# Performance work log

Hardware: AMD Instinct MI355X
Metric: run time of the kernel (lower is better)

The kernel has to match this reference:

```python
import jax, jax.numpy as jnp
import numpy as np

B, C, H, W = 4, 256, 64, 64
D_STATE, D_CONV, EXPAND = 16, 4, 2
D_INNER = EXPAND * C          # 512
DT_RANK = (C + 15) // 16      # 16 (math.ceil(d_model/16), mamba_ssm default)


def setup_inputs() -> dict:
    key = jax.random.key(0)
    ks = jax.random.split(key, 16)
    s = lambda k, shp, sc=0.02: (jax.random.normal(k, shp, dtype=jnp.float32) * sc)
    inp = {
        "spatial_feat": jax.random.normal(ks[0], (B, C, H, W), dtype=jnp.float32),
        "freq_feat":    jax.random.normal(ks[1], (B, C, H, W), dtype=jnp.float32),
        # fusion proj: Linear(2C -> C)
        "W_proj": s(ks[2], (C, 2 * C)),
        "b_proj": jnp.zeros((C,), jnp.float32),
        # Mamba params (mamba_ssm defaults: bias=False for in/out proj, conv_bias=True)
        "W_in":   s(ks[3], (2 * D_INNER, C)),
        "conv_w": s(ks[4], (D_INNER, 1, D_CONV), 0.1),
        "conv_b": jnp.zeros((D_INNER,), jnp.float32),
        "W_x":    s(ks[5], (DT_RANK + 2 * D_STATE, D_INNER)),
        "W_dt":   s(ks[6], (D_INNER, DT_RANK), 0.1),
        "b_dt":   s(ks[7], (D_INNER,), 0.5),
        "A_log":  jnp.log(jnp.tile(jnp.arange(1, D_STATE + 1, dtype=jnp.float32), (D_INNER, 1))),
        "D":      jnp.ones((D_INNER,), jnp.float32),
        "W_out":  s(ks[8], (C, D_INNER)),
        # LayerNorm
        "ln_gamma": jnp.ones((C,), jnp.float32),
        "ln_beta":  jnp.zeros((C,), jnp.float32),
    }
    return inp


def _mamba(x, W_in, conv_w, conv_b, W_x, W_dt, b_dt, A_log, Dp, W_out):
    # x: [B, L, C]
    Bb, L, _ = x.shape
    xz = jnp.einsum("blc,ec->ble", x, W_in)              # [B,L,2*d_inner]
    u, z = jnp.split(xz, 2, axis=-1)                      # each [B,L,d_inner]
    # causal depthwise conv1d along L
    u_c = jnp.transpose(u, (0, 2, 1))                     # [B,d_inner,L]
    u_c = jax.lax.conv_general_dilated(
        u_c, conv_w, window_strides=(1,), padding=[(D_CONV - 1, 0)],
        dimension_numbers=("NCH", "OIH", "NCH"), feature_group_count=D_INNER)
    u_c = u_c + conv_b[None, :, None]
    u = jax.nn.silu(jnp.transpose(u_c, (0, 2, 1)))        # [B,L,d_inner]
    # input-dependent dt, B, C
    dbc = jnp.einsum("bld,rd->blr", u, W_x)               # [B,L,dt_rank+2*d_state]
    dt = dbc[..., :DT_RANK]
    Bm = dbc[..., DT_RANK:DT_RANK + D_STATE]              # [B,L,d_state]
    Cm = dbc[..., DT_RANK + D_STATE:]                     # [B,L,d_state]
    delta = jax.nn.softplus(jnp.einsum("blr,dr->bld", dt, W_dt) + b_dt)  # [B,L,d_inner]
    A = -jnp.exp(A_log)                                   # [d_inner,d_state]

    def step(h, t):
        delta_t, B_t, C_t, u_t = t                        # [B,di],[B,ds],[B,ds],[B,di]
        dA = jnp.exp(delta_t[..., None] * A)              # [B,di,ds]
        h = h * dA + (delta_t * u_t)[..., None] * B_t[:, None, :]
        y = jnp.einsum("bds,bs->bd", h, C_t)
        return h, y

    tm = lambda a: jnp.swapaxes(a, 0, 1)                  # [B,L,..] -> [L,B,..]
    h0 = jnp.zeros((Bb, D_INNER, D_STATE), x.dtype)
    _, ys = jax.lax.scan(step, h0, (tm(delta), tm(Bm), tm(Cm), tm(u)))
    y = jnp.swapaxes(ys, 0, 1)                            # [B,L,d_inner]
    y = y + u * Dp
    y = y * jax.nn.silu(z)
    return jnp.einsum("bld,cd->blc", y, W_out)            # [B,L,C]


def reference(spatial_feat, freq_feat, W_proj, b_proj, W_in, conv_w, conv_b,
              W_x, W_dt, b_dt, A_log, D, W_out, ln_gamma, ln_beta):
    Bb, Cc, Hh, Ww = spatial_feat.shape
    L = Hh * Ww
    xs = jnp.transpose(spatial_feat.reshape(Bb, Cc, L), (0, 2, 1))  # [B,L,C]
    xf = jnp.transpose(freq_feat.reshape(Bb, Cc, L), (0, 2, 1))
    x_cat = jnp.concatenate([xs, xf], axis=-1)                       # [B,L,2C]
    x_proj = jnp.einsum("ble,ce->blc", x_cat, W_proj) + b_proj       # [B,L,C]
    x_mixed = _mamba(x_proj, W_in, conv_w, conv_b, W_x, W_dt, b_dt, A_log, D, W_out)
    mu = jnp.mean(x_mixed, axis=-1, keepdims=True)
    var = jnp.var(x_mixed, axis=-1, keepdims=True)
    x_out = (x_mixed - mu) * jax.lax.rsqrt(var + 1e-5) * ln_gamma + ln_beta
    return jnp.transpose(x_out, (0, 2, 1)).reshape(Bb, Cc, Hh, Ww)
```

## Files before the change

### kernel.cpp

```cpp
#include <hip/hip_runtime.h>
#include <hip/hip_fp16.h>
#include <math.h>

#define L 4096
#define CDIM 256
#define DIN 512
#define DSTATE 16
#define DTR 16
#define BATCH 4

using f32x4  = __attribute__((ext_vector_type(4))) float;
using f16x8  = __attribute__((ext_vector_type(8))) _Float16;

#define LOG2E 1.44269504088896f

#if __has_builtin(__builtin_amdgcn_exp2f)
#define EXP2(x) __builtin_amdgcn_exp2f(x)
#else
#define EXP2(x) __expf((x) * 0.69314718056f)
#endif

__device__ __forceinline__ float silu_f(float x) {
    return __fdividef(x, 1.f + __expf(-x));
}
__device__ __forceinline__ float softplus_fast(float x) {
    return (x > 20.f) ? x : __logf(1.f + __expf(x));
}
__device__ __forceinline__ unsigned pk2h(float a, float b) {
    __half2 h = __floats2half2_rn(a, b);
    return *reinterpret_cast<unsigned*>(&h);
}

#define LDK 40

enum { HEPI_XP = 0, HEPI_UZ = 1, HEPI_F32 = 2, HEPI_D34 = 3 };
template<int EPI, bool A_F32KM, int NT>
__global__ __launch_bounds__(256)
void hgemm(const float* __restrict__ Af0, const float* __restrict__ Af1,
           const __half* __restrict__ Ah_g, const __half* __restrict__ Bh_g,
           const float* __restrict__ bias,
           float* __restrict__ O0, __half* __restrict__ Oh0, __half* __restrict__ Oh1,
           float* __restrict__ Ob, float* __restrict__ Oc,
           int M, int N, int K, int kSplit, long strideAb, int nBlk)
{
    constexpr int BM = 64, MT = 2;
    constexpr int BN = 2 * NT * 16;
    constexpr int BSEG = BN / 64;
    __shared__ __align__(16) _Float16 Ah[2][BM][LDK];
    __shared__ __align__(16) _Float16 Bh[2][BN][LDK];
    const int mBlk = M / BM;
    const int bid = blockIdx.x;
    const int r = bid & 7, q = bid >> 3;
    const int ni = q % nBlk;
    const int mg = (q / nBlk) * 8 + r;
    const int b = mg / mBlk, m_idx = mg - b * mBlk;
    const int n0 = ni * BN, m0 = m_idx * BM;
    const int tid  = threadIdx.x;
    const int lane = tid & 63;
    const int w    = tid >> 6;
    const int wr   = w >> 1, wc = w & 1;
    const int lrow = lane & 15;
    const int loct = lane >> 4;

    f32x4 acc[MT][NT];
    #pragma unroll
    for (int i = 0; i < MT; ++i)
        #pragma unroll
        for (int j = 0; j < NT; ++j)
            acc[i][j] = (f32x4){0.f, 0.f, 0.f, 0.f};

    const int sOct = tid & 3, sRow = tid >> 2;
    float va[8];
    uint4 pa, pb[BSEG];

    auto loadA = [&](int kk) {
        if (A_F32KM) {
            int m = tid & 63, ks = tid >> 6;
            #pragma unroll
            for (int j = 0; j < 8; ++j) {
                int kg = kk + ks * 8 + j;
                const float* Ap; int kl;
                if (kg < kSplit) { Ap = Af0; kl = kg; } else { Ap = Af1; kl = kg - kSplit; }
                va[j] = Ap[(long)b * strideAb + (long)kl * M + m0 + m];
            }
        } else {
            pa = *(const uint4*)(Ah_g + (long)b * strideAb +
                                 (long)(m0 + sRow) * K + kk + sOct * 8);
        }
    };
    auto loadB = [&](int kk) {
        #pragma unroll
        for (int p = 0; p < BSEG; ++p) {
            int ng = n0 + sRow + p * 64;
            if (EPI == HEPI_D34 && ng >= N)
                pb[p] = make_uint4(0, 0, 0, 0);
            else
                pb[p] = *(const uint4*)(Bh_g + (long)ng * K + kk + sOct * 8);
        }
    };
    auto storeAB = [&](int buf) {
        if (A_F32KM) {
            int m = tid & 63, ks = tid >> 6;
            uint4 h;
            h.x = pk2h(va[0], va[1]);
            h.y = pk2h(va[2], va[3]);
            h.z = pk2h(va[4], va[5]);
            h.w = pk2h(va[6], va[7]);
            *(uint4*)&Ah[buf][m][ks * 8] = h;
        } else {
            *(uint4*)&Ah[buf][sRow][sOct * 8] = pa;
        }
        #pragma unroll
        for (int p = 0; p < BSEG; ++p)
            *(uint4*)&Bh[buf][sRow + p * 64][sOct * 8] = pb[p];
    };

    loadA(0); loadB(0);
    storeAB(0);
    __syncthreads();
    int cur = 0;
    for (int kk = 0; kk < K; kk += 32) {
        const bool more = (kk + 32 < K);
        if (more) { loadA(kk + 32); loadB(kk + 32); }
        f16x8 bh[NT];
        #pragma unroll
        for (int nt = 0; nt < NT; ++nt)
            bh[nt] = *(const f16x8*)&Bh[cur][wc*NT*16 + nt*16 + lrow][loct*8];
        #pragma unroll
        for (int mt = 0; mt < MT; ++mt) {
            f16x8 ah = *(const f16x8*)&Ah[cur][wr*MT*16 + mt*16 + lrow][loct*8];
            #pragma unroll
            for (int nt = 0; nt < NT; ++nt)
                acc[mt][nt] = __builtin_amdgcn_mfma_f32_16x16x32_f16(ah, bh[nt], acc[mt][nt], 0, 0, 0);
        }
        if (more) {
            storeAB(cur ^ 1);
            __syncthreads();
            cur ^= 1;
        }
    }
    #pragma unroll
    for (int mt = 0; mt < MT; ++mt) {
        #pragma unroll
        for (int r4 = 0; r4 < 4; ++r4) {
            int m = m0 + wr*MT*16 + mt * 16 + loct * 4 + r4;
            long rowb = (long)b * M + m;
            #pragma unroll
            for (int nt = 0; nt < NT; ++nt) {
                int n = n0 + wc*NT*16 + nt * 16 + lrow;
                float v = acc[mt][nt][r4];
                if (EPI == HEPI_XP) {
                    Oh0[rowb * N + n] = __float2half(v + bias[n]);
                } else if (EPI == HEPI_UZ) {
                    if (n < DIN) Oh0[rowb * DIN + n] = __float2half(v);
                    else         Oh1[rowb * DIN + (n - DIN)] = __float2half(v);
                } else if (EPI == HEPI_D34) {
                    if (n < DTR)           O0[rowb * DTR + n] = v;
                    else if (n < 2 * DTR)  Ob[rowb * 16 + (n - DTR)] = v;
                    else if (n < 48)       Oc[rowb * 16 + (n - 32)] = v;
                } else {
                    O0[rowb * N + n] = v;
                }
            }
        }
    }
}

#define SZ_WP  131072
#define SZ_WIN 262144
#define SZ_WO  131072
#define SZ_WC  24576
__global__ __launch_bounds__(256)
void pack_all(const float* __restrict__ Wp, const float* __restrict__ Win,
              const float* __restrict__ Wout, const float* __restrict__ Wx,
              __half* __restrict__ wph, __half* __restrict__ winh,
              __half* __restrict__ woh, __half* __restrict__ wch)
{
    int i = blockIdx.x * 256 + threadIdx.x;
    if (i < SZ_WP) { wph[i] = __float2half(Wp[i]); return; }
    i -= SZ_WP;
    if (i < SZ_WIN) { winh[i] = __float2half(Win[i]); return; }
    i -= SZ_WIN;
    if (i < SZ_WO) { woh[i] = __float2half(Wout[i]); return; }
    i -= SZ_WO;
    if (i < SZ_WC) wch[i] = __float2half(Wx[i]);
}

__global__ __launch_bounds__(256)
void conv_silu_kernel(const __half* __restrict__ u_pre, const float* __restrict__ cw,
                      const float* __restrict__ cb, __half* __restrict__ u)
{
    long idx = (long)blockIdx.x * blockDim.x + threadIdx.x;
    int d = (int)(idx % DIN);
    long bl = idx / DIN;
    int l = (int)(bl % L);
    long brow = bl - l;
    float v = cb[d];
    #pragma unroll
    for (int j = 0; j < 4; ++j) {
        int li = l - 3 + j;
        if (li >= 0) v += __half2float(u_pre[(brow + li) * DIN + d]) * cw[d * 4 + j];
    }
    u[idx] = __float2half(silu_f(v));
}

#define NC 128
#define LC (L / NC)

__global__ __launch_bounds__(256)
void scan_phase1(const float* __restrict__ dtA, const __half* __restrict__ u,
                 const float* __restrict__ Bm, const float* __restrict__ A_log,
                 const float* __restrict__ Wdt, const float* __restrict__ bdt,
                 float* __restrict__ AX)
{
    __shared__ float sB[LC][DSTATE];
    __shared__ float sDt[LC][DTR];
    __shared__ __half sU[LC][256];
    const int gd = blockIdx.x & 1;
    const int c  = (blockIdx.x >> 1) & (NC - 1);
    const int b  = blockIdx.x >> 8;
    const int tid = threadIdx.x;
    const int d  = gd * 256 + tid;
    const int t0 = c * LC;
    float Arow[DSTATE];
    #pragma unroll
    for (int q = 0; q < 4; ++q) {
        float4 v = *(const float4*)&A_log[d * DSTATE + q * 4];
        Arow[q * 4 + 0] = -__expf(v.x) * LOG2E;
        Arow[q * 4 + 1] = -__expf(v.y) * LOG2E;
        Arow[q * 4 + 2] = -__expf(v.z) * LOG2E;
        Arow[q * 4 + 3] = -__expf(v.w) * LOG2E;
    }
    const float4 W0 = *(const float4*)&Wdt[d * DTR + 0];
    const float4 W1 = *(const float4*)&Wdt[d * DTR + 4];
    const float4 W2 = *(const float4*)&Wdt[d * DTR + 8];
    const float4 W3 = *(const float4*)&Wdt[d * DTR + 12];
    const float bd = bdt[d];
    {
        const __half* ub = u + ((long)b * L + t0) * DIN + gd * 256;
        #pragma unroll
        for (int j = 0; j < 4; ++j) {
            int i = tid + j * 256;
            int t = i >> 5, col = (i & 31) * 8;
            *(float4*)&sU[t][col] = *(const float4*)&ub[(long)t * DIN + col];
        }
        if (tid < 128) {
            const float* Bb = Bm  + ((long)b * L + t0) * DSTATE;
            const float* Db = dtA + ((long)b * L + t0) * DTR;
            *(float4*)&((float*)sB)[tid * 4]  = *(const float4*)&Bb[tid * 4];
            *(float4*)&((float*)sDt)[tid * 4] = *(const float4*)&Db[tid * 4];
        }
    }
    __syncthreads();
    float P[DSTATE], X[DSTATE];
    #pragma unroll
    for (int s = 0; s < DSTATE; ++s) { P[s] = 1.f; X[s] = 0.f; }
    #pragma unroll 2
    for (int t = 0; t < LC; ++t) {
        float4 q0 = *(const float4*)&sDt[t][0];
        float4 q1 = *(const float4*)&sDt[t][4];
        float4 q2 = *(const float4*)&sDt[t][8];
        float4 q3 = *(const float4*)&sDt[t][12];
        float dp0 = fmaf(q0.x, W0.x, fmaf(q0.y, W0.y, fmaf(q0.z, W0.z, q0.w * W0.w)));
        float dp1 = fmaf(q1.x, W1.x, fmaf(q1.y, W1.y, fmaf(q1.z, W1.z, q1.w * W1.w)));
        float dp2 = fmaf(q2.x, W2.x, fmaf(q2.y, W2.y, fmaf(q2.z, W2.z, q2.w * W2.w)));
        float dp3 = fmaf(q3.x, W3.x, fmaf(q3.y, W3.y, fmaf(q3.z, W3.z, q3.w * W3.w)));
        float dlt = softplus_fast(((dp0 + dp1) + (dp2 + dp3)) + bd);
        float du  = dlt * __half2float(sU[t][tid]);
        float Brow[DSTATE];
        *(float4*)&Brow[0]  = *(const float4*)&sB[t][0];
        *(float4*)&Brow[4]  = *(const float4*)&sB[t][4];
        *(float4*)&Brow[8]  = *(const float4*)&sB[t][8];
        *(float4*)&Brow[12] = *(const float4*)&sB[t][12];
        #pragma unroll
        for (int s = 0; s < DSTATE; ++s) {
            float a = EXP2(dlt * Arow[s]);
            P[s] *= a;
            X[s] = fmaf(a, X[s], du * Brow[s]);
        }
    }
    long o2 = ((((long)b * NC + c) * DIN + d) * DSTATE) * 2;
    #pragma unroll
    for (int q = 0; q < 8; ++q)
        *(float4*)&AX[o2 + q * 4] =
            make_float4(P[2*q], X[2*q], P[2*q+1], X[2*q+1]);
}

__global__ __launch_bounds__(256)
void scan_phase2(const float* __restrict__ AX, float* __restrict__ Hout)
{
    int lane = blockIdx.x * 256 + threadIdx.x;
    int b = lane >> 13;
    int rem = lane & 8191;
    const long cs = (long)DIN * DSTATE;
    const long base = (long)b * NC * cs + rem;
    float h = 0.f;
    float2 c0, c1, c2, c3, n0, n1, n2, n3;
    auto ld = [&](int c) -> float2 {
        return *(const float2*)&AX[2 * (base + (long)c * cs)];
    };
    c0 = ld(0); c1 = ld(1); c2 = ld(2); c3 = ld(3);
    n0 = ld(4); n1 = ld(5); n2 = ld(6); n3 = ld(7);
    for (int c = 0; c < NC; c += 4) {
        Hout[base + (long)(c+0) * cs] = h; h = fmaf(c0.x, h, c0.y);
        Hout[base + (long)(c+1) * cs] = h; h = fmaf(c1.x, h, c1.y);
        Hout[base + (long)(c+2) * cs] = h; h = fmaf(c2.x, h, c2.y);
        Hout[base + (long)(c+3) * cs] = h; h = fmaf(c3.x, h, c3.y);
        c0 = n0; c1 = n1; c2 = n2; c3 = n3;
        if (c + 8 < NC) { n0 = ld(c+8); n1 = ld(c+9); n2 = ld(c+10); n3 = ld(c+11); }
    }
}

__global__ __launch_bounds__(256)
void scan_phase3(const float* __restrict__ dtA, const __half* __restrict__ u,
                 const float* __restrict__ Bm, const float* __restrict__ Cm,
                 const __half* __restrict__ z, const float* __restrict__ A_log,
                 const float* __restrict__ Wdt, const float* __restrict__ bdt,
                 const float* __restrict__ Dp, const float* __restrict__ Hinit,
                 __half* __restrict__ y2h)
{
    __shared__ float sB[LC][DSTATE], sC[LC][DSTATE];
    __shared__ float sDt[LC][DTR];
    __shared__ __half sU[LC][256];
    __shared__ __half sZ[LC][256];
    const int gd = blockIdx.x & 1;
    const int c  = (blockIdx.x >> 1) & (NC - 1);
    const int b  = blockIdx.x >> 8;
    const int tid = threadIdx.x;
    const int d  = gd * 256 + tid;
    const int t0 = c * LC;
    float Arow[DSTATE];
    #pragma unroll
    for (int q = 0; q < 4; ++q) {
        float4 v = *(const float4*)&A_log[d * DSTATE + q * 4];
        Arow[q * 4 + 0] = -__expf(v.x) * LOG2E;
        Arow[q * 4 + 1] = -__expf(v.y) * LOG2E;
        Arow[q * 4 + 2] = -__expf(v.z) * LOG2E;
        Arow[q * 4 + 3] = -__expf(v.w) * LOG2E;
    }
    const float4 W0 = *(const float4*)&Wdt[d * DTR + 0];
    const float4 W1 = *(const float4*)&Wdt[d * DTR + 4];
    const float4 W2 = *(const float4*)&Wdt[d * DTR + 8];
    const float4 W3 = *(const float4*)&Wdt[d * DTR + 12];
    const float bd = bdt[d];
    {
        const __half* ub = u + ((long)b * L + t0) * DIN + gd * 256;
        const __half* zb = z + ((long)b * L + t0) * DIN + gd * 256;
        #pragma unroll
        for (int j = 0; j < 4; ++j) {
            int i = tid + j * 256;
            int t = i >> 5, col = (i & 31) * 8;
            *(float4*)&sU[t][col] = *(const float4*)&ub[(long)t * DIN + col];
            *(float4*)&sZ[t][col] = *(const float4*)&zb[(long)t * DIN + col];
        }
        if (tid < 128) {
            const float* Bb = Bm  + ((long)b * L + t0) * DSTATE;
            const float* Cb = Cm  + ((long)b * L + t0) * DSTATE;
            const float* Db = dtA + ((long)b * L + t0) * DTR;
            *(float4*)&((float*)sB)[tid * 4]  = *(const float4*)&Bb[tid * 4];
            *(float4*)&((float*)sC)[tid * 4]  = *(const float4*)&Cb[tid * 4];
            *(float4*)&((float*)sDt)[tid * 4] = *(const float4*)&Db[tid * 4];
        }
    }
    float h[DSTATE];
    {
        long o = (((long)b * NC + c) * DIN + d) * DSTATE;
        #pragma unroll
        for (int q = 0; q < 4; ++q) {
            float4 v = *(const float4*)&Hinit[o + q * 4];
            h[q * 4 + 0] = v.x; h[q * 4 + 1] = v.y;
            h[q * 4 + 2] = v.z; h[q * 4 + 3] = v.w;
        }
    }
    const float Dval = Dp[d];
    __syncthreads();
    #pragma unroll 2
    for (int t = 0; t < LC; ++t) {
        float4 q0 = *(const float4*)&sDt[t][0];
        float4 q1 = *(const float4*)&sDt[t][4];
        float4 q2 = *(const float4*)&sDt[t][8];
        float4 q3 = *(const float4*)&sDt[t][12];
        float dp0 = fmaf(q0.x, W0.x, fmaf(q0.y, W0.y, fmaf(q0.z, W0.z, q0.w * W0.w)));
        float dp1 = fmaf(q1.x, W1.x, fmaf(q1.y, W1.y, fmaf(q1.z, W1.z, q1.w * W1.w)));
        float dp2 = fmaf(q2.x, W2.x, fmaf(q2.y, W2.y, fmaf(q2.z, W2.z, q2.w * W2.w)));
        float dp3 = fmaf(q3.x, W3.x, fmaf(q3.y, W3.y, fmaf(q3.z, W3.z, q3.w * W3.w)));
        float dlt = softplus_fast(((dp0 + dp1) + (dp2 + dp3)) + bd);
        float uu = __half2float(sU[t][tid]);
        float zz = __half2float(sZ[t][tid]);
        float du = dlt * uu;
        float Brow[DSTATE], Crow[DSTATE];
        *(float4*)&Brow[0]  = *(const float4*)&sB[t][0];
        *(float4*)&Brow[4]  = *(const float4*)&sB[t][4];
        *(float4*)&Brow[8]  = *(const float4*)&sB[t][8];
        *(float4*)&Brow[12] = *(const float4*)&sB[t][12];
        *(float4*)&Crow[0]  = *(const float4*)&sC[t][0];
        *(float4*)&Crow[4]  = *(const float4*)&sC[t][4];
        *(float4*)&Crow[8]  = *(const float4*)&sC[t][8];
        *(float4*)&Crow[12] = *(const float4*)&sC[t][12];
        float y0 = 0.f, y1 = 0.f, y2 = 0.f, y3 = 0.f;
        #pragma unroll
        for (int s = 0; s < DSTATE; s += 4) {
            float a0 = EXP2(dlt * Arow[s+0]);
            float a1 = EXP2(dlt * Arow[s+1]);
            float a2 = EXP2(dlt * Arow[s+2]);
            float a3 = EXP2(dlt * Arow[s+3]);
            h[s+0] = fmaf(h[s+0], a0, du * Brow[s+0]);
            h[s+1] = fmaf(h[s+1], a1, du * Brow[s+1]);
            h[s+2] = fmaf(h[s+2], a2, du * Brow[s+2]);
            h[s+3] = fmaf(h[s+3], a3, du * Brow[s+3]);
            y0 = fmaf(h[s+0], Crow[s+0], y0);
            y1 = fmaf(h[s+1], Crow[s+1], y1);
            y2 = fmaf(h[s+2], Crow[s+2], y2);
            y3 = fmaf(h[s+3], Crow[s+3], y3);
        }
        float y = (y0 + y1) + (y2 + y3);
        long gidx = ((long)b * L + t0 + t) * DIN + d;
        y2h[gidx] = __float2half((y + uu * Dval) * silu_f(zz));
    }
}

__global__ __launch_bounds__(256)
void ln_kernel(const float* __restrict__ X, const float* __restrict__ gamma,
               const float* __restrict__ beta, float* __restrict__ out)
{
    __shared__ float tile[32][257];
    __shared__ float sMu[32], sRs[32];
    const int l0 = blockIdx.x * 32;
    const int b  = blockIdx.y;
    const int tid = threadIdx.x;
    for (int i = tid; i < 32 * 256; i += 256) {
        int l = i >> 8, c = i & 255;
        tile[l][c] = X[((long)b * L + l0 + l) * CDIM + c];
    }
    __syncthreads();
    {
        int l = tid >> 3, sub = tid & 7;
        float s1 = 0.f, s2 = 0.f;
        for (int c = sub * 32; c < sub * 32 + 32; ++c) {
            float v = tile[l][c];
            s1 += v; s2 += v * v;
        }
        s1 += __shfl_xor(s1, 1); s2 += __shfl_xor(s2, 1);
        s1 += __shfl_xor(s1, 2); s2 += __shfl_xor(s2, 2);
        s1 += __shfl_xor(s1, 4); s2 += __shfl_xor(s2, 4);
        if (sub == 0) {
            float mu = s1 * (1.f / 256.f);
            float var = s2 * (1.f / 256.f) - mu * mu;
            sMu[l] = mu;
            sRs[l] = rsqrtf(var + 1e-5f);
        }
    }
    __syncthreads();
    for (int i = tid; i < 32 * 256; i += 256) {
        int ll = i & 31, c = i >> 5;
        float v = (tile[ll][c] - sMu[ll]) * sRs[ll] * gamma[c] + beta[c];
        out[((long)b * CDIM + c) * L + l0 + ll] = v;
    }
}

extern "C" void kernel_launch(void* const* d_in, const int* in_sizes, int n_in,
                              void* d_out, int out_size, void* d_ws, size_t ws_size,
                              hipStream_t stream)
{
    const float* sp   = (const float*)d_in[0];
    const float* fq   = (const float*)d_in[1];
    const float* Wp   = (const float*)d_in[2];
    const float* bp   = (const float*)d_in[3];
    const float* Win  = (const float*)d_in[4];
    const float* cw   = (const float*)d_in[5];
    const float* cb   = (const float*)d_in[6];
    const float* Wx   = (const float*)d_in[7];
    const float* Wdt  = (const float*)d_in[8];
    const float* bdt  = (const float*)d_in[9];
    const float* Alog = (const float*)d_in[10];
    const float* Dp   = (const float*)d_in[11];
    const float* Wout = (const float*)d_in[12];
    const float* gam  = (const float*)d_in[13];
    const float* bet  = (const float*)d_in[14];
    float* out = (float*)d_out;
    float* ws  = (float*)d_ws;

    const size_t NLD = (size_t)BATCH * L * DIN;
    const size_t NLC = (size_t)BATCH * L * CDIM;

    size_t off = 0;
    __half* u16   = (__half*)(ws + off); off += NLD / 2;
    __half* u16c  = (__half*)(ws + off); off += NLD / 2;
    __half* z16   = (__half*)(ws + off); off += NLD / 2;
    __half* y16   = (__half*)(ws + off); off += NLD / 2;
    __half* xp16  = (__half*)(ws + off); off += NLC / 2;
    float*  xmix  = ws + off; off += NLC;
    float*  dtA   = ws + off; off += (size_t)BATCH * L * DTR;
    __half* wph   = (__half*)(ws + off); off += SZ_WP / 2;
    __half* winh  = (__half*)(ws + off); off += SZ_WIN / 2;
    __half* woh   = (__half*)(ws + off); off += SZ_WO / 2;
    __half* wch   = (__half*)(ws + off); off += SZ_WC / 2;
    float*  Bmb   = ws + off; off += (size_t)BATCH * L * DSTATE;
    float*  Cmb   = ws + off; off += (size_t)BATCH * L * DSTATE;
    float*  AX    = ws + off; off += (size_t)BATCH * NC * DIN * DSTATE * 2;
    float*  Hout  = ws + off; off += (size_t)BATCH * NC * DIN * DSTATE;

    dim3 blk(256);
    pack_all<<<dim3((SZ_WP + SZ_WIN + SZ_WO + SZ_WC) / 256), blk, 0, stream>>>(
        Wp, Win, Wout, Wx, wph, winh, woh, wch);

    hgemm<HEPI_XP, true, 2><<<dim3(BATCH * (L/64) * 4), blk, 0, stream>>>(
        sp, fq, nullptr, wph, bp, nullptr, xp16, nullptr, nullptr, nullptr,
        L, CDIM, 2 * CDIM, CDIM, (long)CDIM * L, 4);
    hgemm<HEPI_UZ, false, 4><<<dim3(BATCH * (L/64) * 8), blk, 0, stream>>>(
        nullptr, nullptr, xp16, winh, nullptr, nullptr, u16, z16, nullptr, nullptr,
        L, 2 * DIN, CDIM, 1 << 30, (long)L * CDIM, 8);
    conv_silu_kernel<<<dim3((int)(NLD / 256)), blk, 0, stream>>>(u16, cw, cb, u16c);
    hgemm<HEPI_D34, false, 2><<<dim3(BATCH * (L/64) * 1), blk, 0, stream>>>(
        nullptr, nullptr, u16c, wch, nullptr, dtA, nullptr, nullptr, Bmb, Cmb,
        L, 48, DIN, 1 << 30, (long)L * DIN, 1);

    scan_phase1<<<dim3(BATCH * NC * 2), blk, 0, stream>>>(
        dtA, u16c, Bmb, Alog, Wdt, bdt, AX);
    scan_phase2<<<dim3(BATCH * DIN * DSTATE / 256), blk, 0, stream>>>(AX, Hout);
    scan_phase3<<<dim3(BATCH * NC * 2), blk, 0, stream>>>(
        dtA, u16c, Bmb, Cmb, z16, Alog, Wdt, bdt, Dp, Hout, y16);

    hgemm<HEPI_F32, false, 2><<<dim3(BATCH * (L/64) * 4), blk, 0, stream>>>(
        nullptr, nullptr, y16, woh, nullptr, xmix, nullptr, nullptr, nullptr, nullptr,
        L, CDIM, DIN, 1 << 30, (long)L * DIN, 4);
    ln_kernel<<<dim3(L / 32, BATCH), blk, 0, stream>>>(xmix, gam, bet, out);
}
```

Measured before the change: 333.8 us.

## Fold projection weights into in_proj and use power recurrence for integer-ratio A

Multiplies W_in by W_proj at runtime so the fusion projection and in_proj become one GEMM over the raw inputs with a folded bias. This removes the xp16 intermediate and one GEMM pass over L. In both scan kernels, a per-channel check detects A rows that are integer multiples of the first entry. For those rows, one exp2 plus repeated multiplication replaces 16 exp2 per step. Phase 1 also derives the chunk decay product from the summed delta instead of a running product, with some added rounding error from the fp16 folded weights and the power chain.

```diff
diff --git a/kernel.cpp b/kernel.cpp
--- a/kernel.cpp
+++ b/kernel.cpp
@@ -33,7 +33,7 @@
 
 #define LDK 40
 
-enum { HEPI_XP = 0, HEPI_UZ = 1, HEPI_F32 = 2, HEPI_D34 = 3 };
+enum { HEPI_H16 = 0, HEPI_UZ = 1, HEPI_F32 = 2, HEPI_D34 = 3 };
 template<int EPI, bool A_F32KM, int NT>
 __global__ __launch_bounds__(256)
 void hgemm(const float* __restrict__ Af0, const float* __restrict__ Af1,
@@ -149,11 +149,12 @@
             for (int nt = 0; nt < NT; ++nt) {
                 int n = n0 + wc*NT*16 + nt * 16 + lrow;
                 float v = acc[mt][nt][r4];
-                if (EPI == HEPI_XP) {
-                    Oh0[rowb * N + n] = __float2half(v + bias[n]);
+                if (EPI == HEPI_H16) {
+                    Oh0[rowb * N + n] = __float2half(v);
                 } else if (EPI == HEPI_UZ) {
-                    if (n < DIN) Oh0[rowb * DIN + n] = __float2half(v);
-                    else         Oh1[rowb * DIN + (n - DIN)] = __float2half(v);
+                    float vb = v + bias[n];
+                    if (n < DIN) Oh0[rowb * DIN + n] = __float2half(vb);
+                    else         Oh1[rowb * DIN + (n - DIN)] = __float2half(vb);
                 } else if (EPI == HEPI_D34) {
                     if (n < DTR)           O0[rowb * DTR + n] = v;
                     else if (n < 2 * DTR)  Ob[rowb * 16 + (n - DTR)] = v;
@@ -166,24 +167,37 @@
     }
 }
 
-#define SZ_WP  131072
+#define SZ_WPT 131072
 #define SZ_WIN 262144
 #define SZ_WO  131072
 #define SZ_WC  24576
+#define SZ_BF  1024
 __global__ __launch_bounds__(256)
 void pack_all(const float* __restrict__ Wp, const float* __restrict__ Win,
               const float* __restrict__ Wout, const float* __restrict__ Wx,
-              __half* __restrict__ wph, __half* __restrict__ winh,
-              __half* __restrict__ woh, __half* __restrict__ wch)
+              const float* __restrict__ bp,
+              __half* __restrict__ wpt, __half* __restrict__ winh,
+              __half* __restrict__ woh, __half* __restrict__ wch,
+              float* __restrict__ bf)
 {
     int i = blockIdx.x * 256 + threadIdx.x;
-    if (i < SZ_WP) { wph[i] = __float2half(Wp[i]); return; }
-    i -= SZ_WP;
+    if (i < SZ_WPT) {
+        wpt[i] = __float2half(Wp[(i & 255) * 512 + (i >> 8)]);
+        return;
+    }
+    i -= SZ_WPT;
     if (i < SZ_WIN) { winh[i] = __float2half(Win[i]); return; }
     i -= SZ_WIN;
     if (i < SZ_WO) { woh[i] = __float2half(Wout[i]); return; }
     i -= SZ_WO;
-    if (i < SZ_WC) wch[i] = __float2half(Wx[i]);
+    if (i < SZ_WC) { wch[i] = __float2half(Wx[i]); return; }
+    i -= SZ_WC;
+    if (i < SZ_BF) {
+        float acc = 0.f;
+        for (int c = 0; c < CDIM; ++c)
+            acc = fmaf(Win[i * CDIM + c], bp[c], acc);
+        bf[i] = acc;
+    }
 }
 
 __global__ __launch_bounds__(256)
@@ -206,6 +220,12 @@
 
 #define NC 128
 #define LC (L / NC)
+
+#define POWERS16(r, av) \
+    { av[0]=(r); av[1]=av[0]*av[0]; av[2]=av[1]*av[0]; av[3]=av[1]*av[1]; \
+      av[4]=av[3]*av[0]; av[5]=av[3]*av[1]; av[6]=av[3]*av[2]; av[7]=av[3]*av[3]; \
+      av[8]=av[7]*av[0]; av[9]=av[7]*av[1]; av[10]=av[7]*av[2]; av[11]=av[7]*av[3]; \
+      av[12]=av[7]*av[4]; av[13]=av[7]*av[5]; av[14]=av[7]*av[6]; av[15]=av[7]*av[7]; }
 
 __global__ __launch_bounds__(256)
 void scan_phase1(const float* __restrict__ dtA, const __half* __restrict__ u,
@@ -231,6 +251,11 @@
         Arow[q * 4 + 2] = -__expf(v.z) * LOG2E;
         Arow[q * 4 + 3] = -__expf(v.w) * LOG2E;
     }
+    bool intA = true;
+    #pragma unroll
+    for (int s = 1; s < DSTATE; ++s)
+        intA = intA && (fabsf(Arow[s] - (float)(s + 1) * Arow[0]) <= 1e-3f * (float)(s + 1));
+    const float A0L = Arow[0];
     const float4 W0 = *(const float4*)&Wdt[d * DTR + 0];
     const float4 W1 = *(const float4*)&Wdt[d * DTR + 4];
     const float4 W2 = *(const float4*)&Wdt[d * DTR + 8];
@@ -252,33 +277,55 @@
         }
     }
     __syncthreads();
-    float P[DSTATE], X[DSTATE];
-    #pragma unroll
-    for (int s = 0; s < DSTATE; ++s) { P[s] = 1.f; X[s] = 0.f; }
-    #pragma unroll 2
-    for (int t = 0; t < LC; ++t) {
-        float4 q0 = *(const float4*)&sDt[t][0];
-        float4 q1 = *(const float4*)&sDt[t][4];
-        float4 q2 = *(const float4*)&sDt[t][8];
-        float4 q3 = *(const float4*)&sDt[t][12];
-        float dp0 = fmaf(q0.x, W0.x, fmaf(q0.y, W0.y, fmaf(q0.z, W0.z, q0.w * W0.w)));
-        float dp1 = fmaf(q1.x, W1.x, fmaf(q1.y, W1.y, fmaf(q1.z, W1.z, q1.w * W1.w)));
-        float dp2 = fmaf(q2.x, W2.x, fmaf(q2.y, W2.y, fmaf(q2.z, W2.z, q2.w * W2.w)));
-        float dp3 = fmaf(q3.x, W3.x, fmaf(q3.y, W3.y, fmaf(q3.z, W3.z, q3.w * W3.w)));
-        float dlt = softplus_fast(((dp0 + dp1) + (dp2 + dp3)) + bd);
-        float du  = dlt * __half2float(sU[t][tid]);
-        float Brow[DSTATE];
-        *(float4*)&Brow[0]  = *(const float4*)&sB[t][0];
-        *(float4*)&Brow[4]  = *(const float4*)&sB[t][4];
-        *(float4*)&Brow[8]  = *(const float4*)&sB[t][8];
+    float X[DSTATE];
+    #pragma unroll
+    for (int s = 0; s < DSTATE; ++s) X[s] = 0.f;
+    float dsum = 0.f;
+
+#define P1_HEAD \
+        float4 q0 = *(const float4*)&sDt[t][0]; \
+        float4 q1 = *(const float4*)&sDt[t][4]; \
+        float4 q2 = *(const float4*)&sDt[t][8]; \
+        float4 q3 = *(const float4*)&sDt[t][12]; \
+        float dp0 = fmaf(q0.x, W0.x, fmaf(q0.y, W0.y, fmaf(q0.z, W0.z, q0.w * W0.w))); \
+        float dp1 = fmaf(q1.x, W1.x, fmaf(q1.y, W1.y, fmaf(q1.z, W1.z, q1.w * W1.w))); \
+        float dp2 = fmaf(q2.x, W2.x, fmaf(q2.y, W2.y, fmaf(q2.z, W2.z, q2.w * W2.w))); \
+        float dp3 = fmaf(q3.x, W3.x, fmaf(q3.y, W3.y, fmaf(q3.z, W3.z, q3.w * W3.w))); \
+        float dlt = softplus_fast(((dp0 + dp1) + (dp2 + dp3)) + bd); \
+        dsum += dlt; \
+        float du = dlt * __half2float(sU[t][tid]); \
+        float Brow[DSTATE]; \
+        *(float4*)&Brow[0]  = *(const float4*)&sB[t][0]; \
+        *(float4*)&Brow[4]  = *(const float4*)&sB[t][4]; \
+        *(float4*)&Brow[8]  = *(const float4*)&sB[t][8]; \
         *(float4*)&Brow[12] = *(const float4*)&sB[t][12];
-        #pragma unroll
-        for (int s = 0; s < DSTATE; ++s) {
-            float a = EXP2(dlt * Arow[s]);
-            P[s] *= a;
-            X[s] = fmaf(a, X[s], du * Brow[s]);
-        }
-    }
+
+    if (intA) {
+        #pragma unroll 2
+        for (int t = 0; t < LC; ++t) {
+            P1_HEAD
+            float av[DSTATE];
+            float rr = EXP2(dlt * A0L);
+            POWERS16(rr, av)
+            #pragma unroll
+            for (int s = 0; s < DSTATE; ++s)
+                X[s] = fmaf(av[s], X[s], du * Brow[s]);
+        }
+    } else {
+        #pragma unroll 2
+        for (int t = 0; t < LC; ++t) {
+            P1_HEAD
+            #pragma unroll
+            for (int s = 0; s < DSTATE; ++s) {
+                float a = EXP2(dlt * Arow[s]);
+                X[s] = fmaf(a, X[s], du * Brow[s]);
+            }
+        }
+    }
+#undef P1_HEAD
+    float P[DSTATE];
+    #pragma unroll
+    for (int s = 0; s < DSTATE; ++s) P[s] = EXP2(dsum * Arow[s]);
     long o2 = ((((long)b * NC + c) * DIN + d) * DSTATE) * 2;
     #pragma unroll
     for (int q = 0; q < 8; ++q)
@@ -338,6 +385,11 @@
         Arow[q * 4 + 2] = -__expf(v.z) * LOG2E;
         Arow[q * 4 + 3] = -__expf(v.w) * LOG2E;
     }
+    bool intA = true;
+    #pragma unroll
+    for (int s = 1; s < DSTATE; ++s)
+        intA = intA && (fabsf(Arow[s] - (float)(s + 1) * Arow[0]) <= 1e-3f * (float)(s + 1));
+    const float A0L = Arow[0];
     const float4 W0 = *(const float4*)&Wdt[d * DTR + 0];
     const float4 W1 = *(const float4*)&Wdt[d * DTR + 4];
     const float4 W2 = *(const float4*)&Wdt[d * DTR + 8];
@@ -373,50 +425,70 @@
         }
     }
     const float Dval = Dp[d];
+    const long gbase = ((long)b * L + t0) * DIN + d;
     __syncthreads();
-    #pragma unroll 2
-    for (int t = 0; t < LC; ++t) {
-        float4 q0 = *(const float4*)&sDt[t][0];
-        float4 q1 = *(const float4*)&sDt[t][4];
-        float4 q2 = *(const float4*)&sDt[t][8];
-        float4 q3 = *(const float4*)&sDt[t][12];
-        float dp0 = fmaf(q0.x, W0.x, fmaf(q0.y, W0.y, fmaf(q0.z, W0.z, q0.w * W0.w)));
-        float dp1 = fmaf(q1.x, W1.x, fmaf(q1.y, W1.y, fmaf(q1.z, W1.z, q1.w * W1.w)));
-        float dp2 = fmaf(q2.x, W2.x, fmaf(q2.y, W2.y, fmaf(q2.z, W2.z, q2.w * W2.w)));
-        float dp3 = fmaf(q3.x, W3.x, fmaf(q3.y, W3.y, fmaf(q3.z, W3.z, q3.w * W3.w)));
-        float dlt = softplus_fast(((dp0 + dp1) + (dp2 + dp3)) + bd);
-        float uu = __half2float(sU[t][tid]);
-        float zz = __half2float(sZ[t][tid]);
-        float du = dlt * uu;
-        float Brow[DSTATE], Crow[DSTATE];
-        *(float4*)&Brow[0]  = *(const float4*)&sB[t][0];
-        *(float4*)&Brow[4]  = *(const float4*)&sB[t][4];
-        *(float4*)&Brow[8]  = *(const float4*)&sB[t][8];
-        *(float4*)&Brow[12] = *(const float4*)&sB[t][12];
-        *(float4*)&Crow[0]  = *(const float4*)&sC[t][0];
-        *(float4*)&Crow[4]  = *(const float4*)&sC[t][4];
-        *(float4*)&Crow[8]  = *(const float4*)&sC[t][8];
+
+#define P3_HEAD \
+        float4 q0 = *(const float4*)&sDt[t][0]; \
+        float4 q1 = *(const float4*)&sDt[t][4]; \
+        float4 q2 = *(const float4*)&sDt[t][8]; \
+        float4 q3 = *(const float4*)&sDt[t][12]; \
+        float dp0 = fmaf(q0.x, W0.x, fmaf(q0.y, W0.y, fmaf(q0.z, W0.z, q0.w * W0.w))); \
+        float dp1 = fmaf(q1.x, W1.x, fmaf(q1.y, W1.y, fmaf(q1.z, W1.z, q1.w * W1.w))); \
+        float dp2 = fmaf(q2.x, W2.x, fmaf(q2.y, W2.y, fmaf(q2.z, W2.z, q2.w * W2.w))); \
+        float dp3 = fmaf(q3.x, W3.x, fmaf(q3.y, W3.y, fmaf(q3.z, W3.z, q3.w * W3.w))); \
+        float dlt = softplus_fast(((dp0 + dp1) + (dp2 + dp3)) + bd); \
+        float uu = __half2float(sU[t][tid]); \
+        float zz = __half2float(sZ[t][tid]); \
+        float du = dlt * uu; \
+        float Brow[DSTATE], Crow[DSTATE]; \
+        *(float4*)&Brow[0]  = *(const float4*)&sB[t][0]; \
+        *(float4*)&Brow[4]  = *(const float4*)&sB[t][4]; \
+        *(float4*)&Brow[8]  = *(const float4*)&sB[t][8]; \
+        *(float4*)&Brow[12] = *(const float4*)&sB[t][12]; \
+        *(float4*)&Crow[0]  = *(const float4*)&sC[t][0]; \
+        *(float4*)&Crow[4]  = *(const float4*)&sC[t][4]; \
+        *(float4*)&Crow[8]  = *(const float4*)&sC[t][8]; \
         *(float4*)&Crow[12] = *(const float4*)&sC[t][12];
-        float y0 = 0.f, y1 = 0.f, y2 = 0.f, y3 = 0.f;
-        #pragma unroll
-        for (int s = 0; s < DSTATE; s += 4) {
-            float a0 = EXP2(dlt * Arow[s+0]);
-            float a1 = EXP2(dlt * Arow[s+1]);
-            float a2 = EXP2(dlt * Arow[s+2]);
-            float a3 = EXP2(dlt * Arow[s+3]);
-            h[s+0] = fmaf(h[s+0], a0, du * Brow[s+0]);
-            h[s+1] = fmaf(h[s+1], a1, du * Brow[s+1]);
-            h[s+2] = fmaf(h[s+2], a2, du * Brow[s+2]);
-            h[s+3] = fmaf(h[s+3], a3, du * Brow[s+3]);
-            y0 = fmaf(h[s+0], Crow[s+0], y0);
-            y1 = fmaf(h[s+1], Crow[s+1], y1);
-            y2 = fmaf(h[s+2], Crow[s+2], y2);
-            y3 = fmaf(h[s+3], Crow[s+3], y3);
-        }
-        float y = (y0 + y1) + (y2 + y3);
-        long gidx = ((long)b * L + t0 + t) * DIN + d;
-        y2h[gidx] = __float2half((y + uu * Dval) * silu_f(zz));
-    }
+
+#define P3_TAIL(AV) \
+        float y0 = 0.f, y1 = 0.f, y2 = 0.f, y3 = 0.f; \
+        _Pragma("unroll") \
+        for (int s = 0; s < DSTATE; s += 4) { \
+            h[s+0] = fmaf(h[s+0], AV(s+0), du * Brow[s+0]); \
+            h[s+1] = fmaf(h[s+1], AV(s+1), du * Brow[s+1]); \
+            h[s+2] = fmaf(h[s+2], AV(s+2), du * Brow[s+2]); \
+            h[s+3] = fmaf(h[s+3], AV(s+3), du * Brow[s+3]); \
+            y0 = fmaf(h[s+0], Crow[s+0], y0); \
+            y1 = fmaf(h[s+1], Crow[s+1], y1); \
+            y2 = fmaf(h[s+2], Crow[s+2], y2); \
+            y3 = fmaf(h[s+3], Crow[s+3], y3); \
+        } \
+        float y = (y0 + y1) + (y2 + y3); \
+        y2h[gbase + t * DIN] = __float2half((y + uu * Dval) * silu_f(zz));
+
+    if (intA) {
+        #pragma unroll 2
+        for (int t = 0; t < LC; ++t) {
+            P3_HEAD
+            float av[DSTATE];
+            float rr = EXP2(dlt * A0L);
+            POWERS16(rr, av)
+            #define AVF(s) av[s]
+            P3_TAIL(AVF)
+            #undef AVF
+        }
+    } else {
+        #pragma unroll 2
+        for (int t = 0; t < LC; ++t) {
+            P3_HEAD
+            #define AVG(s) EXP2(dlt * Arow[s])
+            P3_TAIL(AVG)
+            #undef AVG
+        }
+    }
+#undef P3_HEAD
+#undef P3_TAIL
 }
 
 __global__ __launch_bounds__(256)
@@ -488,28 +560,31 @@
     __half* u16c  = (__half*)(ws + off); off += NLD / 2;
     __half* z16   = (__half*)(ws + off); off += NLD / 2;
     __half* y16   = (__half*)(ws + off); off += NLD / 2;
-    __half* xp16  = (__half*)(ws + off); off += NLC / 2;
     float*  xmix  = ws + off; off += NLC;
     float*  dtA   = ws + off; off += (size_t)BATCH * L * DTR;
-    __half* wph   = (__half*)(ws + off); off += SZ_WP / 2;
+    __half* wpt   = (__half*)(ws + off); off += SZ_WPT / 2;
     __half* winh  = (__half*)(ws + off); off += SZ_WIN / 2;
     __half* woh   = (__half*)(ws + off); off += SZ_WO / 2;
     __half* wch   = (__half*)(ws + off); off += SZ_WC / 2;
+    __half* wfh   = (__half*)(ws + off); off += (size_t)1024 * 512 / 2;
+    float*  bf    = ws + off; off += SZ_BF;
     float*  Bmb   = ws + off; off += (size_t)BATCH * L * DSTATE;
     float*  Cmb   = ws + off; off += (size_t)BATCH * L * DSTATE;
     float*  AX    = ws + off; off += (size_t)BATCH * NC * DIN * DSTATE * 2;
     float*  Hout  = ws + off; off += (size_t)BATCH * NC * DIN * DSTATE;
 
     dim3 blk(256);
-    pack_all<<<dim3((SZ_WP + SZ_WIN + SZ_WO + SZ_WC) / 256), blk, 0, stream>>>(
-        Wp, Win, Wout, Wx, wph, winh, woh, wch);
-
-    hgemm<HEPI_XP, true, 2><<<dim3(BATCH * (L/64) * 4), blk, 0, stream>>>(
-        sp, fq, nullptr, wph, bp, nullptr, xp16, nullptr, nullptr, nullptr,
-        L, CDIM, 2 * CDIM, CDIM, (long)CDIM * L, 4);
-    hgemm<HEPI_UZ, false, 4><<<dim3(BATCH * (L/64) * 8), blk, 0, stream>>>(
-        nullptr, nullptr, xp16, winh, nullptr, nullptr, u16, z16, nullptr, nullptr,
-        L, 2 * DIN, CDIM, 1 << 30, (long)L * CDIM, 8);
+    pack_all<<<dim3((SZ_WPT + SZ_WIN + SZ_WO + SZ_WC + SZ_BF) / 256), blk, 0, stream>>>(
+        Wp, Win, Wout, Wx, bp, wpt, winh, woh, wch, bf);
+
+    hgemm<HEPI_H16, false, 4><<<dim3(64), blk, 0, stream>>>(
+        nullptr, nullptr, winh, wpt, nullptr, nullptr, wfh, nullptr, nullptr, nullptr,
+        1024, 512, 256, 1 << 30, (long)1024 * 256, 4);
+
+    hgemm<HEPI_UZ, true, 4><<<dim3(BATCH * (L/64) * 8), blk, 0, stream>>>(
+        sp, fq, nullptr, wfh, bf, nullptr, u16, z16, nullptr, nullptr,
+        L, 2 * DIN, 2 * CDIM, CDIM, (long)CDIM * L, 8);
+
     conv_silu_kernel<<<dim3((int)(NLD / 256)), blk, 0, stream>>>(u16, cw, cb, u16c);
     hgemm<HEPI_D34, false, 2><<<dim3(BATCH * (L/64) * 1), blk, 0, stream>>>(
         nullptr, nullptr, u16c, wch, nullptr, dtA, nullptr, nullptr, Bmb, Cmb,
```

New measurement: 359.6 us. 1.08x slower.

## Use 128x128 GEMM tiles for dense projections and derive scan decay from delta sum

Applied to the files above, without the earlier changes.

Adds a 128x128-tile MFMA GEMM kernel with 4x4 fragments per wave and uses it for the fusion projection, the in-projection and the out-projection. Larger tiles give more reuse per shared-memory load, in exchange for fewer blocks and higher register pressure. Scan phase 1 also drops the running product of per-step decays and instead computes the chunk decay once as exp2 of the summed delta times A. This removes 16 multiplies per step but changes rounding slightly.

```diff
diff --git a/kernel.cpp b/kernel.cpp
--- a/kernel.cpp
+++ b/kernel.cpp
@@ -33,7 +33,134 @@
 
 #define LDK 40
 
+
 enum { HEPI_XP = 0, HEPI_UZ = 1, HEPI_F32 = 2, HEPI_D34 = 3 };
+
+template<int EPI, bool A_F32KM>
+__global__ __launch_bounds__(256)
+void hgemm128(const float* __restrict__ Af0, const float* __restrict__ Af1,
+              const __half* __restrict__ Ah_g, const __half* __restrict__ Bh_g,
+              const float* __restrict__ bias,
+              float* __restrict__ O0, __half* __restrict__ Oh0, __half* __restrict__ Oh1,
+              int M, int N, int K, int kSplit, long strideAb, int nBlk)
+{
+    constexpr int BM = 128, BN = 128, MT = 4, NT = 4;
+    __shared__ __align__(16) _Float16 Ah[2][BM][LDK];
+    __shared__ __align__(16) _Float16 Bh[2][BN][LDK];
+    const int mBlk = M / BM;
+    const int bid = blockIdx.x;
+    const int r = bid & 7, q = bid >> 3;
+    const int ni = q % nBlk;
+    const int mg = (q / nBlk) * 8 + r;
+    const int b = mg / mBlk, m_idx = mg - b * mBlk;
+    const int n0 = ni * BN, m0 = m_idx * BM;
+    const int tid  = threadIdx.x;
+    const int lane = tid & 63;
+    const int w    = tid >> 6;
+    const int wr   = w >> 1, wc = w & 1;
+    const int lrow = lane & 15;
+    const int loct = lane >> 4;
+
+    f32x4 acc[MT][NT];
+    #pragma unroll
+    for (int i = 0; i < MT; ++i)
+        #pragma unroll
+        for (int j = 0; j < NT; ++j)
+            acc[i][j] = (f32x4){0.f, 0.f, 0.f, 0.f};
+
+    const int sOct = tid & 3, sRow = tid >> 2;
+    float va[16];
+    uint4 pa[2], pb[2];
+
+    auto loadA = [&](int kk) {
+        if (A_F32KM) {
+            int m = tid & 127, kh = (tid >> 7) * 16;
+            #pragma unroll
+            for (int j = 0; j < 16; ++j) {
+                int kg = kk + kh + j;
+                const float* Ap; int kl;
+                if (kg < kSplit) { Ap = Af0; kl = kg; } else { Ap = Af1; kl = kg - kSplit; }
+                va[j] = Ap[(long)b * strideAb + (long)kl * M + m0 + m];
+            }
+        } else {
+            #pragma unroll
+            for (int p = 0; p < 2; ++p)
+                pa[p] = *(const uint4*)(Ah_g + (long)b * strideAb +
+                                        (long)(m0 + sRow + p * 64) * K + kk + sOct * 8);
+        }
+    };
+    auto loadB = [&](int kk) {
+        #pragma unroll
+        for (int p = 0; p < 2; ++p)
+            pb[p] = *(const uint4*)(Bh_g + (long)(n0 + sRow + p * 64) * K + kk + sOct * 8);
+    };
+    auto storeAB = [&](int buf) {
+        if (A_F32KM) {
+            int m = tid & 127, kh = (tid >> 7) * 16;
+            uint4 h0, h1;
+            h0.x = pk2h(va[0], va[1]);   h0.y = pk2h(va[2], va[3]);
+            h0.z = pk2h(va[4], va[5]);   h0.w = pk2h(va[6], va[7]);
+            h1.x = pk2h(va[8], va[9]);   h1.y = pk2h(va[10], va[11]);
+            h1.z = pk2h(va[12], va[13]); h1.w = pk2h(va[14], va[15]);
+            *(uint4*)&Ah[buf][m][kh]     = h0;
+            *(uint4*)&Ah[buf][m][kh + 8] = h1;
+        } else {
+            #pragma unroll
+            for (int p = 0; p < 2; ++p)
+                *(uint4*)&Ah[buf][sRow + p * 64][sOct * 8] = pa[p];
+        }
+        #pragma unroll
+        for (int p = 0; p < 2; ++p)
+            *(uint4*)&Bh[buf][sRow + p * 64][sOct * 8] = pb[p];
+    };
+
+    loadA(0); loadB(0);
+    storeAB(0);
+    __syncthreads();
+    int cur = 0;
+    for (int kk = 0; kk < K; kk += 32) {
+        const bool more = (kk + 32 < K);
+        if (more) { loadA(kk + 32); loadB(kk + 32); }
+        f16x8 bh[NT];
+        #pragma unroll
+        for (int nt = 0; nt < NT; ++nt)
+            bh[nt] = *(const f16x8*)&Bh[cur][wc*64 + nt*16 + lrow][loct*8];
+        #pragma unroll
+        for (int mt = 0; mt < MT; ++mt) {
+            f16x8 ah = *(const f16x8*)&Ah[cur][wr*64 + mt*16 + lrow][loct*8];
+            #pragma unroll
+            for (int nt = 0; nt < NT; ++nt)
+                acc[mt][nt] = __builtin_amdgcn_mfma_f32_16x16x32_f16(ah, bh[nt], acc[mt][nt], 0, 0, 0);
+        }
+        if (more) {
+            storeAB(cur ^ 1);
+            __syncthreads();
+            cur ^= 1;
+        }
+    }
+    #pragma unroll
+    for (int mt = 0; mt < MT; ++mt) {
+        #pragma unroll
+        for (int r4 = 0; r4 < 4; ++r4) {
+            int m = m0 + wr*64 + mt * 16 + loct * 4 + r4;
+            long rowb = (long)b * M + m;
+            #pragma unroll
+            for (int nt = 0; nt < NT; ++nt) {
+                int n = n0 + wc*64 + nt * 16 + lrow;
+                float v = acc[mt][nt][r4];
+                if (EPI == HEPI_XP) {
+                    Oh0[rowb * N + n] = __float2half(v + bias[n]);
+                } else if (EPI == HEPI_UZ) {
+                    if (n < DIN) Oh0[rowb * DIN + n] = __float2half(v);
+                    else         Oh1[rowb * DIN + (n - DIN)] = __float2half(v);
+                } else {
+                    O0[rowb * N + n] = v;
+                }
+            }
+        }
+    }
+}
+
 template<int EPI, bool A_F32KM, int NT>
 __global__ __launch_bounds__(256)
 void hgemm(const float* __restrict__ Af0, const float* __restrict__ Af1,
@@ -70,23 +197,11 @@
             acc[i][j] = (f32x4){0.f, 0.f, 0.f, 0.f};
 
     const int sOct = tid & 3, sRow = tid >> 2;
-    float va[8];
     uint4 pa, pb[BSEG];
 
     auto loadA = [&](int kk) {
-        if (A_F32KM) {
-            int m = tid & 63, ks = tid >> 6;
-            #pragma unroll
-            for (int j = 0; j < 8; ++j) {
-                int kg = kk + ks * 8 + j;
-                const float* Ap; int kl;
-                if (kg < kSplit) { Ap = Af0; kl = kg; } else { Ap = Af1; kl = kg - kSplit; }
-                va[j] = Ap[(long)b * strideAb + (long)kl * M + m0 + m];
-            }
-        } else {
-            pa = *(const uint4*)(Ah_g + (long)b * strideAb +
-                                 (long)(m0 + sRow) * K + kk + sOct * 8);
-        }
+        pa = *(const uint4*)(Ah_g + (long)b * strideAb +
+                             (long)(m0 + sRow) * K + kk + sOct * 8);
     };
     auto loadB = [&](int kk) {
         #pragma unroll
@@ -99,17 +214,7 @@
         }
     };
     auto storeAB = [&](int buf) {
-        if (A_F32KM) {
-            int m = tid & 63, ks = tid >> 6;
-            uint4 h;
-            h.x = pk2h(va[0], va[1]);
-            h.y = pk2h(va[2], va[3]);
-            h.z = pk2h(va[4], va[5]);
-            h.w = pk2h(va[6], va[7]);
-            *(uint4*)&Ah[buf][m][ks * 8] = h;
-        } else {
-            *(uint4*)&Ah[buf][sRow][sOct * 8] = pa;
-        }
+        *(uint4*)&Ah[buf][sRow][sOct * 8] = pa;
         #pragma unroll
         for (int p = 0; p < BSEG; ++p)
             *(uint4*)&Bh[buf][sRow + p * 64][sOct * 8] = pb[p];
@@ -149,12 +254,7 @@
             for (int nt = 0; nt < NT; ++nt) {
                 int n = n0 + wc*NT*16 + nt * 16 + lrow;
                 float v = acc[mt][nt][r4];
-                if (EPI == HEPI_XP) {
-                    Oh0[rowb * N + n] = __float2half(v + bias[n]);
-                } else if (EPI == HEPI_UZ) {
-                    if (n < DIN) Oh0[rowb * DIN + n] = __float2half(v);
-                    else         Oh1[rowb * DIN + (n - DIN)] = __float2half(v);
-                } else if (EPI == HEPI_D34) {
+                if (EPI == HEPI_D34) {
                     if (n < DTR)           O0[rowb * DTR + n] = v;
                     else if (n < 2 * DTR)  Ob[rowb * 16 + (n - DTR)] = v;
                     else if (n < 48)       Oc[rowb * 16 + (n - 32)] = v;
@@ -252,9 +352,10 @@
         }
     }
     __syncthreads();
-    float P[DSTATE], X[DSTATE];
-    #pragma unroll
-    for (int s = 0; s < DSTATE; ++s) { P[s] = 1.f; X[s] = 0.f; }
+    float X[DSTATE];
+    #pragma unroll
+    for (int s = 0; s < DSTATE; ++s) X[s] = 0.f;
+    float dsum = 0.f;
     #pragma unroll 2
     for (int t = 0; t < LC; ++t) {
         float4 q0 = *(const float4*)&sDt[t][0];
@@ -266,6 +367,7 @@
         float dp2 = fmaf(q2.x, W2.x, fmaf(q2.y, W2.y, fmaf(q2.z, W2.z, q2.w * W2.w)));
         float dp3 = fmaf(q3.x, W3.x, fmaf(q3.y, W3.y, fmaf(q3.z, W3.z, q3.w * W3.w)));
         float dlt = softplus_fast(((dp0 + dp1) + (dp2 + dp3)) + bd);
+        dsum += dlt;
         float du  = dlt * __half2float(sU[t][tid]);
         float Brow[DSTATE];
         *(float4*)&Brow[0]  = *(const float4*)&sB[t][0];
@@ -275,10 +377,12 @@
         #pragma unroll
         for (int s = 0; s < DSTATE; ++s) {
             float a = EXP2(dlt * Arow[s]);
-            P[s] *= a;
             X[s] = fmaf(a, X[s], du * Brow[s]);
         }
     }
+    float P[DSTATE];
+    #pragma unroll
+    for (int s = 0; s < DSTATE; ++s) P[s] = EXP2(dsum * Arow[s]);
     long o2 = ((((long)b * NC + c) * DIN + d) * DSTATE) * 2;
     #pragma unroll
     for (int q = 0; q < 8; ++q)
@@ -504,12 +608,13 @@
     pack_all<<<dim3((SZ_WP + SZ_WIN + SZ_WO + SZ_WC) / 256), blk, 0, stream>>>(
         Wp, Win, Wout, Wx, wph, winh, woh, wch);
 
-    hgemm<HEPI_XP, true, 2><<<dim3(BATCH * (L/64) * 4), blk, 0, stream>>>(
-        sp, fq, nullptr, wph, bp, nullptr, xp16, nullptr, nullptr, nullptr,
-        L, CDIM, 2 * CDIM, CDIM, (long)CDIM * L, 4);
-    hgemm<HEPI_UZ, false, 4><<<dim3(BATCH * (L/64) * 8), blk, 0, stream>>>(
-        nullptr, nullptr, xp16, winh, nullptr, nullptr, u16, z16, nullptr, nullptr,
+    hgemm128<HEPI_XP, true><<<dim3(BATCH * (L/128) * 2), blk, 0, stream>>>(
+        sp, fq, nullptr, wph, bp, nullptr, xp16, nullptr,
+        L, CDIM, 2 * CDIM, CDIM, (long)CDIM * L, 2);
+    hgemm128<HEPI_UZ, false><<<dim3(BATCH * (L/128) * 8), blk, 0, stream>>>(
+        nullptr, nullptr, xp16, winh, nullptr, nullptr, u16, z16,
         L, 2 * DIN, CDIM, 1 << 30, (long)L * CDIM, 8);
+
     conv_silu_kernel<<<dim3((int)(NLD / 256)), blk, 0, stream>>>(u16, cw, cb, u16c);
     hgemm<HEPI_D34, false, 2><<<dim3(BATCH * (L/64) * 1), blk, 0, stream>>>(
         nullptr, nullptr, u16c, wch, nullptr, dtA, nullptr, nullptr, Bmb, Cmb,
@@ -521,8 +626,8 @@
     scan_phase3<<<dim3(BATCH * NC * 2), blk, 0, stream>>>(
         dtA, u16c, Bmb, Cmb, z16, Alog, Wdt, bdt, Dp, Hout, y16);
 
-    hgemm<HEPI_F32, false, 2><<<dim3(BATCH * (L/64) * 4), blk, 0, stream>>>(
-        nullptr, nullptr, y16, woh, nullptr, xmix, nullptr, nullptr, nullptr, nullptr,
-        L, CDIM, DIN, 1 << 30, (long)L * DIN, 4);
+    hgemm128<HEPI_F32, false><<<dim3(BATCH * (L/128) * 2), blk, 0, stream>>>(
+        nullptr, nullptr, y16, woh, nullptr, xmix, nullptr, nullptr,
+        L, CDIM, DIN, 1 << 30, (long)L * DIN, 2);
     ln_kernel<<<dim3(L / 32, BATCH), blk, 0, stream>>>(xmix, gam, bet, out);
 }
```

New measurement: 357.8 us. +7.2%, slower.
